# Kernel tuning notes

Hardware: AMD Instinct MI355X
Metric: run time of the kernel (lower is better)

## Reference

```python
import jax, jax.numpy as jnp
import numpy as np

N, E, H = 5000, 40000, 8
DIMS = [(258, 512), (516, 256), (262, 128), (136, 20)]  # (in_feature, out_feature) per GATDeformer


def setup_inputs() -> dict:
    key = jax.random.key(0)
    ks = jax.random.split(key, 10)
    s = 0.05
    data = jax.random.normal(ks[0], (N, 10), jnp.float32)
    src = jax.random.randint(ks[1], (E,), 0, N)
    off = jax.random.randint(ks[2], (E,), 1, N)
    edge_idx = jnp.stack([src, (src + off) % N]).astype(jnp.int32)  # no self loops by construction
    inp = {
        'data': data,
        'edge_idx': edge_idx,
        'W0': jax.random.normal(ks[3], (10, 256), jnp.float32) * s,
        'b0': jnp.zeros((256,), jnp.float32),
    }
    for i, (din, dout) in enumerate(DIMS, start=1):
        k = jax.random.split(ks[3 + i], 3)
        inp[f'W{i}'] = jax.random.normal(k[0], (din, H * dout), jnp.float32) * s
        inp[f'asrc{i}'] = jax.random.normal(k[1], (H, dout), jnp.float32) * s
        inp[f'adst{i}'] = jax.random.normal(k[2], (H, dout), jnp.float32) * s
        inp[f'bias{i}'] = jnp.zeros((dout,), jnp.float32)
    return inp


def _gat(x, src, dst, W, a_s, a_d, b):
    """PyG GATConv (concat=False): returns (mean-over-heads output + bias, alpha [E',H])."""
    Hh, C = a_s.shape
    h = (x @ W).reshape(N, Hh, C)                               # [N,H,C]
    e_s = jnp.einsum('nhc,hc->nh', h, a_s)                      # [N,H]
    e_d = jnp.einsum('nhc,hc->nh', h, a_d)
    logits = jax.nn.leaky_relu(e_s[src] + e_d[dst], 0.2)        # [E',H]
    m = jax.ops.segment_max(logits, dst, num_segments=N)        # segment softmax over incoming edges
    ex = jnp.exp(logits - m[dst])
    alpha = ex / jax.ops.segment_sum(ex, dst, num_segments=N)[dst]
    out = jax.ops.segment_sum(alpha[:, :, None] * h[src], dst, num_segments=N)  # [N,H,C]
    return out.mean(axis=1) + b, alpha


def _deformer(af, src, dst, W, a_s, a_d, b):
    # find_boundary on the layer input features
    up, down = af[:, 0] == 1.0, af[:, 0] == 0.0
    left, right = af[:, 1] == 0.0, af[:, 1] == 1.0
    feat, alpha = _gat(af, src, dst, W, a_s, a_d, b)
    coord = af[:, :2]
    # second propagate: alpha*0.2 reused to aggregate source coordinates, then mean over heads
    msg = (alpha * 0.2)[:, :, None] * coord[src][:, None, :]    # [E',H,2]
    oc = jax.ops.segment_sum(msg, dst, num_segments=N).mean(axis=1)
    # fix_boundary (sequential overwrite order: up then down, left then right)
    c0 = jnp.where(down, 0.0, jnp.where(up, 1.0, oc[:, 0]))
    c1 = jnp.where(right, 1.0, jnp.where(left, 0.0, oc[:, 1]))
    return jnp.stack([c0, c1], axis=1), jax.nn.selu(feat)


def reference(data, edge_idx, W0, b0, W1, asrc1, adst1, bias1, W2, asrc2, adst2, bias2, W3, asrc3, adst3, bias3, W4, asrc4, adst4, bias4):
    sl = jnp.arange(N, dtype=edge_idx.dtype)
    src = jnp.concatenate([edge_idx[0], sl])   # GATConv add_self_loops=True
    dst = jnp.concatenate([edge_idx[1], sl])
    coord = data[:, :2]
    feat = jax.nn.selu(data @ W0 + b0)
    c1_, f1 = _deformer(jnp.concatenate([coord, feat], 1), src, dst, W1, asrc1, adst1, bias1)
    c2_, f2 = _deformer(jnp.concatenate([c1_, coord, f1], 1), src, dst, W2, asrc2, adst2, bias2)
    c3_, f3 = _deformer(jnp.concatenate([c2_, c1_, coord, f2], 1), src, dst, W3, asrc3, adst3, bias3)
    c4_, _ = _deformer(jnp.concatenate([c3_, c2_, c1_, coord, f3], 1), src, dst, W4, asrc4, adst4, bias4)
    return c4_
```

## Files before the change

### kernel.cpp

```cpp
#include <hip/hip_runtime.h>

#define N_NODES 5000
#define NH 8

typedef unsigned short u16;
typedef short bf16x8 __attribute__((ext_vector_type(8)));
typedef float f32x4 __attribute__((ext_vector_type(4)));

static __device__ __forceinline__ float selu_f(float x) {
    const float sc = 1.0507009873554805f;
    const float al = 1.6732632423543772f;
    return x > 0.f ? sc * x : sc * al * (__expf(x) - 1.f);
}

static __device__ __forceinline__ u16 f2bf(float x) {
    union { float f; unsigned u; } v; v.f = x;
    unsigned r = v.u + 0x7fff + ((v.u >> 16) & 1);
    return (u16)(r >> 16);
}

static __device__ __forceinline__ float bf2f(unsigned hi16) {
    union { unsigned u; float f; } v; v.u = hi16 << 16;
    return v.f;
}

#define GL2LDS16(gp, lp)                                                        \
    __builtin_amdgcn_global_load_lds(                                           \
        (const __attribute__((address_space(1))) void*)(gp),                    \
        (__attribute__((address_space(3))) void*)(lp), 16, 0, 0)

__global__ void k_count(const int* __restrict__ ei, int* cnt, int E, int Esz) {
    int e = blockIdx.x * 256 + threadIdx.x;
    if (e >= Esz) return;
    int dst = (e < E) ? ei[E + e] : (e - E);
    atomicAdd(&cnt[dst], 1);
}

__global__ void k_scan(const int* __restrict__ cnt, int* __restrict__ rowp, int n) {
    __shared__ int ps[256];
    int t = threadIdx.x;
    int per = (n + 255) / 256;
    int b = t * per;
    int s = 0;
    for (int i = 0; i < per; ++i) { int idx = b + i; if (idx < n) s += cnt[idx]; }
    ps[t] = s;
    __syncthreads();
    for (int off = 1; off < 256; off <<= 1) {
        int v = (t >= off) ? ps[t - off] : 0;
        __syncthreads();
        ps[t] += v;
        __syncthreads();
    }
    int run = (t == 0) ? 0 : ps[t - 1];
    for (int i = 0; i < per; ++i) {
        int idx = b + i;
        if (idx < n) { rowp[idx] = run; run += cnt[idx]; }
    }
    if (t == 255) rowp[n] = run;
}

__global__ void k_fill(const int* __restrict__ ei, const int* __restrict__ rowp,
                       int* cur, int* ssrc, int E, int Esz) {
    int e = blockIdx.x * 256 + threadIdx.x;
    if (e >= Esz) return;
    int src, dst;
    if (e < E) { src = ei[e]; dst = ei[E + e]; }
    else       { src = e - E; dst = src; }
    int pos = rowp[dst] + atomicAdd(&cur[dst], 1);
    ssrc[pos] = src;
}

__global__ __launch_bounds__(256) void k_prep(
        const float* W1, const float* W2, const float* W3, const float* W4,
        const float* s1, const float* s2, const float* s3, const float* s4,
        const float* d1, const float* d2, const float* d3, const float* d4,
        float* __restrict__ fsAll, float* __restrict__ fdAll,
        u16* T1, u16* T2, u16* T3) {
    const int Ks[4] = {258, 516, 262, 136};
    const int Cs[4] = {512, 256, 128, 20};
    int bid = blockIdx.x;
    if (bid < 516) {
        int li = bid / 129;
        int k = (bid % 129) * 4 + (threadIdx.x >> 6);
        int lane = threadIdx.x & 63;
        if (k >= Ks[li]) return;
        const float* W  = (li == 0) ? W1 : (li == 1) ? W2 : (li == 2) ? W3 : W4;
        const float* as = (li == 0) ? s1 : (li == 1) ? s2 : (li == 2) ? s3 : s4;
        const float* ad = (li == 0) ? d1 : (li == 1) ? d2 : (li == 2) ? d3 : d4;
        int C = Cs[li];
        float s[8] = {0.f,0.f,0.f,0.f,0.f,0.f,0.f,0.f};
        float d[8] = {0.f,0.f,0.f,0.f,0.f,0.f,0.f,0.f};
        const float* wr = W + (size_t)k * 8 * C;
        for (int c = lane; c < C; c += 64) {
            #pragma unroll
            for (int h = 0; h < 8; ++h) {
                float w = wr[h * C + c];
                s[h] += w * as[h * C + c];
                d[h] += w * ad[h * C + c];
            }
        }
        #pragma unroll
        for (int off = 32; off >= 1; off >>= 1) {
            #pragma unroll
            for (int h = 0; h < 8; ++h) {
                s[h] += __shfl_xor(s[h], off);
                d[h] += __shfl_xor(d[h], off);
            }
        }
        if (lane == 0) {
            float* fo = fsAll + (size_t)li * 516 * 8 + k * 8;
            float* go = fdAll + (size_t)li * 516 * 8 + k * 8;
            #pragma unroll
            for (int h = 0; h < 8; ++h) { fo[h] = s[h]; go[h] = d[h]; }
        }
    } else {
        const int Kps[3] = {288, 544, 288};
        int w = bid - 516;
        int li = w / (16 * 136);
        int rem = w % (16 * 136);
        int c0 = (rem % 16) * 32;
        int j0 = (rem / 16) * 32;
        int C = Cs[li], K = Ks[li], Kp = Kps[li], KK = 8 * Kp;
        if (c0 >= C || j0 >= KK) return;
        const float* W = (li == 0) ? W1 : (li == 1) ? W2 : W3;
        u16* Wt2 = (li == 0) ? T1 : (li == 1) ? T2 : T3;
        __shared__ float tile[32][33];
        int h = j0 / Kp, k0 = j0 % Kp;
        int tid = threadIdx.x;
        for (int idx = tid; idx < 1024; idx += 256) {
            int kr = idx >> 5, cc = idx & 31;
            int gk = k0 + kr;
            tile[kr][cc] = (gk < K) ? W[(size_t)gk * (8 * C) + h * C + c0 + cc] : 0.f;
        }
        __syncthreads();
        for (int idx = tid; idx < 1024; idx += 256) {
            int cr = idx >> 5, kc = idx & 31;
            Wt2[(size_t)(c0 + cr) * KK + j0 + kc] = f2bf(tile[kc][cr]);
        }
    }
}

__global__ __launch_bounds__(256) void k_mf(const float* p0, const float* p1,
                                            const float* p2, const float* p3, int np,
                                            const float* __restrict__ data,
                                            const float* __restrict__ W0,
                                            const float* __restrict__ b0,
                                            const u16* __restrict__ facc,
                                            const float* __restrict__ biasp,
                                            int split, int MN, int FC, int K, int Kp,
                                            const float* __restrict__ fs,
                                            const float* __restrict__ fd,
                                            u16* __restrict__ afb,
                                            float* __restrict__ es, float* __restrict__ ed,
                                            float* __restrict__ c0out) {
    int n = blockIdx.x, t = threadIdx.x;
    __shared__ float drow[10];
    bool l1 = (biasp == nullptr);
    if (l1 && t < 10) drow[t] = data[n * 10 + t];
    __syncthreads();
    float pes[8] = {0.f,0.f,0.f,0.f,0.f,0.f,0.f,0.f};
    float ped[8] = {0.f,0.f,0.f,0.f,0.f,0.f,0.f,0.f};
    u16* rowb = afb + (size_t)n * Kp;
    for (int cf = t; cf < FC; cf += 256) {
        float v;
        if (l1) {
            v = b0[cf];
            #pragma unroll
            for (int k = 0; k < 10; ++k) v += drow[k] * W0[k * 256 + cf];
            v = selu_f(v);
        } else {
            float s = 0.f;
            for (int z = 0; z < split; ++z)
                s += bf2f(facc[(size_t)z * MN + (size_t)n * FC + cf]);
            v = selu_f(s * 0.125f + biasp[cf]);
        }
        int c = 2 * np + cf;
        rowb[c] = f2bf(v);
        const float* fsr = fs + c * 8;
        const float* fdr = fd + c * 8;
        #pragma unroll
        for (int h = 0; h < 8; ++h) { pes[h] += v * fsr[h]; ped[h] += v * fdr[h]; }
    }
    if (t < 2 * np) {
        float v;
        if (l1) {
            v = drow[t];
            c0out[n * 2 + t] = v;
        } else {
            const float* p = (t < 2) ? p0 : (t < 4) ? p1 : (t < 6) ? p2 : p3;
            v = p[n * 2 + (t & 1)];
        }
        rowb[t] = f2bf(v);
        #pragma unroll
        for (int h = 0; h < 8; ++h) { pes[h] += v * fs[t * 8 + h]; ped[h] += v * fd[t * 8 + h]; }
    }
    for (int c = K + t; c < Kp; c += 256) rowb[c] = 0;
    #pragma unroll
    for (int off = 32; off >= 1; off >>= 1) {
        #pragma unroll
        for (int h = 0; h < 8; ++h) {
            pes[h] += __shfl_xor(pes[h], off);
            ped[h] += __shfl_xor(ped[h], off);
        }
    }
    __shared__ float red[4][16];
    int wv = t >> 6, ln = t & 63;
    if (ln == 0) {
        #pragma unroll
        for (int h = 0; h < 8; ++h) { red[wv][h] = pes[h]; red[wv][8 + h] = ped[h]; }
    }
    __syncthreads();
    if (t < 16) {
        float s = red[0][t] + red[1][t] + red[2][t] + red[3][t];
        if (t < 8) es[n * 8 + t] = s;
        else       ed[n * 8 + (t - 8)] = s;
    }
}

template <int S32>
__global__ __launch_bounds__(256) void k_gag(const float* __restrict__ es,
                            const float* __restrict__ ed,
                            const int* __restrict__ rowp, const int* __restrict__ ssrc,
                            const float* __restrict__ cprev, const u16* __restrict__ afb,
                            u16* __restrict__ g, float* __restrict__ cnext, int Kp) {
    __shared__ int   ls[128];
    __shared__ float la[128 * 8];
    __shared__ float lc0[128], lc1[128], lw[128];
    __shared__ float linv[8];
    int n = blockIdx.x, t = threadIdx.x;
    int s0 = rowp[n];
    int deg = rowp[n + 1] - s0;
    if (deg > 128) deg = 128;
    for (int i = t; i < deg; i += 256) {
        int src = ssrc[s0 + i];
        ls[i] = src;
        lc0[i] = cprev[src * 2];
        lc1[i] = cprev[src * 2 + 1];
    }
    __syncthreads();
    for (int i = t; i < deg * 8; i += 256) {
        int e = i >> 3, h = i & 7;
        float x = es[ls[e] * 8 + h] + ed[n * 8 + h];
        la[i] = x > 0.f ? x : 0.2f * x;
    }
    __syncthreads();
    if (t < 8) {
        float m = -1e30f;
        for (int e = 0; e < deg; ++e) m = fmaxf(m, la[e * 8 + t]);
        float s = 0.f;
        for (int e = 0; e < deg; ++e) {
            float v = __expf(la[e * 8 + t] - m);
            la[e * 8 + t] = v;
            s += v;
        }
        linv[t] = 1.f / s;
    }
    __syncthreads();
    for (int i = t; i < deg; i += 256) {
        float w = 0.f;
        #pragma unroll
        for (int h = 0; h < 8; ++h) w += la[i * 8 + h] * linv[h];
        lw[i] = w;
    }
    int nW = Kp >> 1;
    float acc[8][2 * S32];
    #pragma unroll
    for (int h = 0; h < 8; ++h)
        #pragma unroll
        for (int s = 0; s < 2 * S32; ++s) acc[h][s] = 0.f;
    int e = 0;
    for (; e + 1 < deg; e += 2) {
        const unsigned* r0 = (const unsigned*)(afb + (size_t)ls[e] * Kp);
        const unsigned* r1 = (const unsigned*)(afb + (size_t)ls[e + 1] * Kp);
        unsigned v0[S32], v1[S32];
        #pragma unroll
        for (int s = 0; s < S32; ++s) {
            int w = t + 256 * s;
            v0[s] = (w < nW) ? r0[w] : 0u;
            v1[s] = (w < nW) ? r1[w] : 0u;
        }
        float a0[8], a1[8];
        #pragma unroll
        for (int h = 0; h < 8; ++h) { a0[h] = la[e * 8 + h]; a1[h] = la[(e + 1) * 8 + h]; }
        #pragma unroll
        for (int s = 0; s < S32; ++s) {
            float x0 = bf2f(v0[s] & 0xffff), y0 = bf2f(v0[s] >> 16);
            float x1 = bf2f(v1[s] & 0xffff), y1 = bf2f(v1[s] >> 16);
            #pragma unroll
            for (int h = 0; h < 8; ++h) {
                acc[h][2 * s]     += a0[h] * x0 + a1[h] * x1;
                acc[h][2 * s + 1] += a0[h] * y0 + a1[h] * y1;
            }
        }
    }
    if (e < deg) {
        const unsigned* r0 = (const unsigned*)(afb + (size_t)ls[e] * Kp);
        unsigned v0[S32];
        #pragma unroll
        for (int s = 0; s < S32; ++s) {
            int w = t + 256 * s;
            v0[s] = (w < nW) ? r0[w] : 0u;
        }
        float a0[8];
        #pragma unroll
        for (int h = 0; h < 8; ++h) a0[h] = la[e * 8 + h];
        #pragma unroll
        for (int s = 0; s < S32; ++s) {
            float x0 = bf2f(v0[s] & 0xffff), y0 = bf2f(v0[s] >> 16);
            #pragma unroll
            for (int h = 0; h < 8; ++h) {
                acc[h][2 * s]     += a0[h] * x0;
                acc[h][2 * s + 1] += a0[h] * y0;
            }
        }
    }
    unsigned* grw = (unsigned*)(g + (size_t)n * 8 * Kp);
    #pragma unroll
    for (int s = 0; s < S32; ++s) {
        int w = t + 256 * s;
        if (w < nW) {
            #pragma unroll
            for (int h = 0; h < 8; ++h) {
                float iv = linv[h];
                unsigned lo = f2bf(acc[h][2 * s] * iv);
                unsigned hi = f2bf(acc[h][2 * s + 1] * iv);
                grw[h * nW + w] = lo | (hi << 16);
            }
        }
    }
    __syncthreads();
    if (t == 0) {
        float oc0 = 0.f, oc1 = 0.f;
        for (int i = 0; i < deg; ++i) { oc0 += lw[i] * lc0[i]; oc1 += lw[i] * lc1[i]; }
        oc0 *= 0.025f; oc1 *= 0.025f;
        float a0 = cprev[n * 2], a1 = cprev[n * 2 + 1];
        cnext[n * 2]     = (a0 == 0.f) ? 0.f : ((a0 == 1.f) ? 1.f : oc0);
        cnext[n * 2 + 1] = (a1 == 1.f) ? 1.f : ((a1 == 0.f) ? 0.f : oc1);
    }
}

__global__ __launch_bounds__(256) void k_gemm_s(const u16* __restrict__ A,
                                                const u16* __restrict__ Bt,
                                                u16* __restrict__ facc16,
                                                int M, int KK, int NC, int kchunk, int MN) {
    __shared__ u16 As[2][128 * 32];
    __shared__ u16 Bs[2][128 * 32];
    int tid = threadIdx.x;
    int wave = tid >> 6, lane = tid & 63;
    int bm = blockIdx.y * 128, bn = blockIdx.x * 128, z = blockIdx.z;
    int kbeg = z * kchunk, kend = min(KK, kbeg + kchunk);
    int wm = (wave >> 1) * 64, wn = (wave & 1) * 64;
    int l16 = lane & 15, q = lane >> 4;
    f32x4 acc[4][4] = {};

    int seg0 = wave * 128 + lane;
    int seg1 = seg0 + 64;
    int row0 = seg0 >> 2, sq0 = (seg0 & 3) ^ (row0 & 3);
    int row1 = seg1 >> 2, sq1 = (seg1 & 3) ^ (row1 & 3);
    const u16* ga0 = A  + (size_t)(bm + row0) * KK + sq0 * 8;
    const u16* ga1 = A  + (size_t)(bm + row1) * KK + sq1 * 8;
    const u16* gb0 = Bt + (size_t)(bn + row0) * KK + sq0 * 8;
    const u16* gb1 = Bt + (size_t)(bn + row1) * KK + sq1 * 8;
    int lo0 = (wave * 2 + 0) * 512;
    int lo1 = (wave * 2 + 1) * 512;

#define STAGE_T(buf, kk)                          \
    do {                                          \
        GL2LDS16(ga0 + (kk), &As[buf][lo0]);      \
        GL2LDS16(ga1 + (kk), &As[buf][lo1]);      \
        GL2LDS16(gb0 + (kk), &Bs[buf][lo0]);      \
        GL2LDS16(gb1 + (kk), &Bs[buf][lo1]);      \
    } while (0)

    STAGE_T(0, kbeg);
    int cur = 0;
    for (int k0 = kbeg; k0 < kend; k0 += 32) {
        if (k0 + 32 < kend) {
            STAGE_T(cur ^ 1, k0 + 32);
            asm volatile("s_waitcnt vmcnt(4)" ::: "memory");
        } else {
            asm volatile("s_waitcnt vmcnt(0)" ::: "memory");
        }
        __builtin_amdgcn_s_barrier();
        const u16* Asr = As[cur];
        const u16* Bsr = Bs[cur];
        bf16x8 fa[4], fb[4];
        #pragma unroll
        for (int mi = 0; mi < 4; ++mi) {
            int row = wm + mi * 16 + l16;
            fa[mi] = *(const bf16x8*)(Asr + row * 32 + ((q ^ (row & 3)) * 8));
            int col = wn + mi * 16 + l16;
            fb[mi] = *(const bf16x8*)(Bsr + col * 32 + ((q ^ (col & 3)) * 8));
        }
        #pragma unroll
        for (int mi = 0; mi < 4; ++mi)
            #pragma unroll
            for (int ni = 0; ni < 4; ++ni)
                acc[mi][ni] = __builtin_amdgcn_mfma_f32_16x16x32_bf16(fa[mi], fb[ni], acc[mi][ni], 0, 0, 0);
        __builtin_amdgcn_s_barrier();
        cur ^= 1;
    }
#undef STAGE_T
    u16* out = facc16 + (size_t)z * MN;
    #pragma unroll
    for (int mi = 0; mi < 4; ++mi) {
        int row0s = bm + wm + mi * 16 + q * 4;
        #pragma unroll
        for (int ni = 0; ni < 4; ++ni) {
            int col = bn + wn + ni * 16 + l16;
            #pragma unroll
            for (int r = 0; r < 4; ++r) {
                int row = row0s + r;
                if (row < M) out[(size_t)row * NC + col] = f2bf(acc[mi][ni][r]);
            }
        }
    }
}

__global__ void k_final(const float* __restrict__ es, const float* __restrict__ ed,
                        const int* __restrict__ rowp, const int* __restrict__ ssrc,
                        const float* __restrict__ cprev, float* __restrict__ outp) {
    int wid = (blockIdx.x * blockDim.x + threadIdx.x) >> 6;
    int lane = threadIdx.x & 63;
    if (wid >= N_NODES) return;
    int n = wid;
    int s0 = rowp[n], deg = rowp[n + 1] - s0;
    int h = lane & 7, ei = lane >> 3;
    float edh = ed[n * 8 + h];
    float m = -1e30f;
    for (int b = 0; b < deg; b += 8) {
        int e = b + ei;
        if (e < deg) {
            int src = ssrc[s0 + e];
            float x = es[src * 8 + h] + edh;
            x = x > 0.f ? x : 0.2f * x;
            m = fmaxf(m, x);
        }
    }
    m = fmaxf(m, __shfl_xor(m, 8));
    m = fmaxf(m, __shfl_xor(m, 16));
    m = fmaxf(m, __shfl_xor(m, 32));
    float ssum = 0.f;
    for (int b = 0; b < deg; b += 8) {
        int e = b + ei;
        if (e < deg) {
            int src = ssrc[s0 + e];
            float x = es[src * 8 + h] + edh;
            x = x > 0.f ? x : 0.2f * x;
            ssum += __expf(x - m);
        }
    }
    ssum += __shfl_xor(ssum, 8);
    ssum += __shfl_xor(ssum, 16);
    ssum += __shfl_xor(ssum, 32);
    float inv = 1.f / ssum;
    float oc0 = 0.f, oc1 = 0.f;
    for (int b = 0; b < deg; b += 8) {
        int e = b + ei;
        if (e < deg) {
            int src = ssrc[s0 + e];
            float x = es[src * 8 + h] + edh;
            x = x > 0.f ? x : 0.2f * x;
            float w = __expf(x - m) * inv;
            w += __shfl_xor(w, 1);
            w += __shfl_xor(w, 2);
            w += __shfl_xor(w, 4);
            if (h == 0) {
                oc0 += w * cprev[src * 2];
                oc1 += w * cprev[src * 2 + 1];
            }
        }
    }
    oc0 += __shfl_xor(oc0, 8);  oc1 += __shfl_xor(oc1, 8);
    oc0 += __shfl_xor(oc0, 16); oc1 += __shfl_xor(oc1, 16);
    oc0 += __shfl_xor(oc0, 32); oc1 += __shfl_xor(oc1, 32);
    if (lane == 0) {
        oc0 *= 0.025f; oc1 *= 0.025f;
        float a0 = cprev[n * 2], a1 = cprev[n * 2 + 1];
        outp[n * 2]     = (a0 == 0.f) ? 0.f : ((a0 == 1.f) ? 1.f : oc0);
        outp[n * 2 + 1] = (a1 == 1.f) ? 1.f : ((a1 == 0.f) ? 0.f : oc1);
    }
}

extern "C" void kernel_launch(void* const* d_in, const int* in_sizes, int n_in,
                              void* d_out, int out_size, void* d_ws, size_t ws_size,
                              hipStream_t stream) {
    const float* data = (const float*)d_in[0];
    const int* ei = (const int*)d_in[1];
    const float* W0 = (const float*)d_in[2];
    const float* b0 = (const float*)d_in[3];
    int E = in_sizes[1] / 2;
    int Esz = E + N_NODES;

    char* wp = (char*)d_ws;
    size_t off = 0;
    auto alloc = [&](size_t bytes) {
        void* p = wp + off;
        off += (bytes + 1023) & ~(size_t)1023;
        return p;
    };
    u16*   g     = (u16*)alloc((size_t)N_NODES * 8 * 576 * 2);
    u16*   T1    = (u16*)alloc((size_t)512 * 8 * 288 * 2);
    u16*   T2    = (u16*)alloc((size_t)256 * 8 * 544 * 2);
    u16*   T3    = (u16*)alloc((size_t)128 * 8 * 288 * 2);
    u16*   facc  = (u16*)alloc((size_t)8 * N_NODES * 512 * 2);
    u16*   afb   = (u16*)alloc((size_t)N_NODES * 576 * 2);
    float* es    = (float*)alloc((size_t)N_NODES * 8 * 4);
    float* ebd   = (float*)alloc((size_t)N_NODES * 8 * 4);
    float* fsAll = (float*)alloc((size_t)4 * 516 * 8 * 4);
    float* fdAll = (float*)alloc((size_t)4 * 516 * 8 * 4);
    float* c0    = (float*)alloc(N_NODES * 2 * 4);
    float* c1    = (float*)alloc(N_NODES * 2 * 4);
    float* c2    = (float*)alloc(N_NODES * 2 * 4);
    float* c3    = (float*)alloc(N_NODES * 2 * 4);
    int* cnt  = (int*)alloc(N_NODES * 2 * 4);
    int* cur  = cnt + N_NODES;
    int* rowp = (int*)alloc((N_NODES + 1) * 4);
    int* ssrc = (int*)alloc(Esz * 4);

    hipMemsetAsync(cnt, 0, N_NODES * 2 * 4, stream);
    int gE = (Esz + 255) / 256;
    k_count<<<gE, 256, 0, stream>>>(ei, cnt, E, Esz);
    k_scan<<<1, 256, 0, stream>>>(cnt, rowp, N_NODES);
    k_fill<<<gE, 256, 0, stream>>>(ei, rowp, cur, ssrc, E, Esz);

    struct LP { const float *W, *as, *ad, *bs; int K, C, split; };
    LP L[4] = {
        {(const float*)d_in[4],  (const float*)d_in[5],  (const float*)d_in[6],  (const float*)d_in[7],  258, 512, 4},
        {(const float*)d_in[8],  (const float*)d_in[9],  (const float*)d_in[10], (const float*)d_in[11], 516, 256, 8},
        {(const float*)d_in[12], (const float*)d_in[13], (const float*)d_in[14], (const float*)d_in[15], 262, 128, 8},
        {(const float*)d_in[16], (const float*)d_in[17], (const float*)d_in[18], (const float*)d_in[19], 136, 20, 1},
    };
    k_prep<<<516 + 16 * 136 * 3, 256, 0, stream>>>(
        L[0].W, L[1].W, L[2].W, L[3].W,
        L[0].as, L[1].as, L[2].as, L[3].as,
        L[0].ad, L[1].ad, L[2].ad, L[3].ad,
        fsAll, fdAll, T1, T2, T3);

    float* cbuf[4] = {c0, c1, c2, c3};
    u16* Tb[3] = {T1, T2, T3};
    int FC[4] = {256, 512, 256, 128};

    for (int li = 0; li < 4; ++li) {
        LP& lp = L[li];
        const float* p[4] = {nullptr, nullptr, nullptr, nullptr};
        for (int j = 0; j <= li; ++j) p[j] = cbuf[li - j];
        int Kp = ((lp.K + 31) / 32) * 32;
        int KK = 8 * Kp;
        const float* biasp = (li == 0) ? nullptr : L[li - 1].bs;
        int splitp = (li == 0) ? 1 : L[li - 1].split;
        int MNp = N_NODES * FC[li];
        const float* fs = fsAll + (size_t)li * 516 * 8;
        const float* fd = fdAll + (size_t)li * 516 * 8;

        k_mf<<<N_NODES, 256, 0, stream>>>(p[0], p[1], p[2], p[3], li + 1,
                                          data, W0, b0, facc, biasp, splitp, MNp, FC[li],
                                          lp.K, Kp, fs, fd, afb, es, ebd, c0);
        if (li < 3) {
            if ((Kp >> 1) <= 256)
                k_gag<1><<<N_NODES, 256, 0, stream>>>(es, ebd, rowp, ssrc, cbuf[li], afb,
                                                      g, cbuf[li + 1], Kp);
            else
                k_gag<2><<<N_NODES, 256, 0, stream>>>(es, ebd, rowp, ssrc, cbuf[li], afb,
                                                      g, cbuf[li + 1], Kp);
            int MN = N_NODES * lp.C;
            k_gemm_s<<<dim3(lp.C / 128, (N_NODES + 127) / 128, lp.split), 256, 0, stream>>>(
                g, Tb[li], facc, N_NODES, KK, lp.C, KK / lp.split, MN);
        } else {
            k_final<<<(N_NODES + 3) / 4, 256, 0, stream>>>(es, ebd, rowp, ssrc, cbuf[3],
                                                           (float*)d_out);
        }
    }
}
```

Before: 369.8 us.

## Triple-buffer GEMM LDS, unroll aggregation by four edges, vectorize feature prep

The GEMM now keeps three LDS stages in flight instead of two, prefetching two k-steps ahead with adjusted vmcnt waits to better hide global-to-LDS latency. The edge aggregation loop processes four neighbor rows per iteration instead of two, raising memory-level parallelism, and the tail becomes a scalar loop. The feature-prep kernel handles two columns per thread with float2/packed bf16 loads and stores. These cost more LDS (lower occupancy risk) and more registers in the aggregation kernel.

```diff
diff --git a/kernel.cpp b/kernel.cpp
--- a/kernel.cpp
+++ b/kernel.cpp
@@ -161,25 +161,39 @@
     float pes[8] = {0.f,0.f,0.f,0.f,0.f,0.f,0.f,0.f};
     float ped[8] = {0.f,0.f,0.f,0.f,0.f,0.f,0.f,0.f};
     u16* rowb = afb + (size_t)n * Kp;
-    for (int cf = t; cf < FC; cf += 256) {
-        float v;
+    for (int cf2 = t; 2 * cf2 < FC; cf2 += 256) {
+        int cf = 2 * cf2;
+        float v0, v1;
         if (l1) {
-            v = b0[cf];
-            #pragma unroll
-            for (int k = 0; k < 10; ++k) v += drow[k] * W0[k * 256 + cf];
-            v = selu_f(v);
+            float2 bb = *(const float2*)(b0 + cf);
+            v0 = bb.x; v1 = bb.y;
+            #pragma unroll
+            for (int k = 0; k < 10; ++k) {
+                float2 ww = *(const float2*)(W0 + k * 256 + cf);
+                v0 += drow[k] * ww.x;
+                v1 += drow[k] * ww.y;
+            }
+            v0 = selu_f(v0); v1 = selu_f(v1);
         } else {
-            float s = 0.f;
-            for (int z = 0; z < split; ++z)
-                s += bf2f(facc[(size_t)z * MN + (size_t)n * FC + cf]);
-            v = selu_f(s * 0.125f + biasp[cf]);
+            float s0 = 0.f, s1 = 0.f;
+            for (int z = 0; z < split; ++z) {
+                unsigned pr = *(const unsigned*)(facc + (size_t)z * MN + (size_t)n * FC + cf);
+                s0 += bf2f(pr & 0xffff);
+                s1 += bf2f(pr >> 16);
+            }
+            float2 bb = *(const float2*)(biasp + cf);
+            v0 = selu_f(s0 * 0.125f + bb.x);
+            v1 = selu_f(s1 * 0.125f + bb.y);
         }
         int c = 2 * np + cf;
-        rowb[c] = f2bf(v);
+        *(unsigned*)(rowb + c) = (unsigned)f2bf(v0) | ((unsigned)f2bf(v1) << 16);
         const float* fsr = fs + c * 8;
         const float* fdr = fd + c * 8;
         #pragma unroll
-        for (int h = 0; h < 8; ++h) { pes[h] += v * fsr[h]; ped[h] += v * fdr[h]; }
+        for (int h = 0; h < 8; ++h) {
+            pes[h] += v0 * fsr[h] + v1 * fsr[8 + h];
+            ped[h] += v0 * fdr[h] + v1 * fdr[8 + h];
+        }
     }
     if (t < 2 * np) {
         float v;
@@ -269,31 +283,43 @@
         #pragma unroll
         for (int s = 0; s < 2 * S32; ++s) acc[h][s] = 0.f;
     int e = 0;
-    for (; e + 1 < deg; e += 2) {
+    for (; e + 3 < deg; e += 4) {
         const unsigned* r0 = (const unsigned*)(afb + (size_t)ls[e] * Kp);
         const unsigned* r1 = (const unsigned*)(afb + (size_t)ls[e + 1] * Kp);
-        unsigned v0[S32], v1[S32];
+        const unsigned* r2 = (const unsigned*)(afb + (size_t)ls[e + 2] * Kp);
+        const unsigned* r3 = (const unsigned*)(afb + (size_t)ls[e + 3] * Kp);
+        unsigned v0[S32], v1[S32], v2[S32], v3[S32];
         #pragma unroll
         for (int s = 0; s < S32; ++s) {
             int w = t + 256 * s;
-            v0[s] = (w < nW) ? r0[w] : 0u;
-            v1[s] = (w < nW) ? r1[w] : 0u;
-        }
-        float a0[8], a1[8];
-        #pragma unroll
-        for (int h = 0; h < 8; ++h) { a0[h] = la[e * 8 + h]; a1[h] = la[(e + 1) * 8 + h]; }
+            bool ok = (w < nW);
+            v0[s] = ok ? r0[w] : 0u;
+            v1[s] = ok ? r1[w] : 0u;
+            v2[s] = ok ? r2[w] : 0u;
+            v3[s] = ok ? r3[w] : 0u;
+        }
+        float a0[8], a1[8], a2[8], a3[8];
+        #pragma unroll
+        for (int h = 0; h < 8; ++h) {
+            a0[h] = la[(e + 0) * 8 + h];
+            a1[h] = la[(e + 1) * 8 + h];
+            a2[h] = la[(e + 2) * 8 + h];
+            a3[h] = la[(e + 3) * 8 + h];
+        }
         #pragma unroll
         for (int s = 0; s < S32; ++s) {
             float x0 = bf2f(v0[s] & 0xffff), y0 = bf2f(v0[s] >> 16);
             float x1 = bf2f(v1[s] & 0xffff), y1 = bf2f(v1[s] >> 16);
+            float x2 = bf2f(v2[s] & 0xffff), y2 = bf2f(v2[s] >> 16);
+            float x3 = bf2f(v3[s] & 0xffff), y3 = bf2f(v3[s] >> 16);
             #pragma unroll
             for (int h = 0; h < 8; ++h) {
-                acc[h][2 * s]     += a0[h] * x0 + a1[h] * x1;
-                acc[h][2 * s + 1] += a0[h] * y0 + a1[h] * y1;
-            }
-        }
-    }
-    if (e < deg) {
+                acc[h][2 * s]     += a0[h] * x0 + a1[h] * x1 + a2[h] * x2 + a3[h] * x3;
+                acc[h][2 * s + 1] += a0[h] * y0 + a1[h] * y1 + a2[h] * y2 + a3[h] * y3;
+            }
+        }
+    }
+    for (; e < deg; ++e) {
         const unsigned* r0 = (const unsigned*)(afb + (size_t)ls[e] * Kp);
         unsigned v0[S32];
         #pragma unroll
@@ -343,8 +369,8 @@
                                                 const u16* __restrict__ Bt,
                                                 u16* __restrict__ facc16,
                                                 int M, int KK, int NC, int kchunk, int MN) {
-    __shared__ u16 As[2][128 * 32];
-    __shared__ u16 Bs[2][128 * 32];
+    __shared__ u16 As[3][128 * 32];
+    __shared__ u16 Bs[3][128 * 32];
     int tid = threadIdx.x;
     int wave = tid >> 6, lane = tid & 63;
     int bm = blockIdx.y * 128, bn = blockIdx.x * 128, z = blockIdx.z;
@@ -373,10 +399,14 @@
     } while (0)
 
     STAGE_T(0, kbeg);
+    if (kbeg + 32 < kend) STAGE_T(1, kbeg + 32);
     int cur = 0;
     for (int k0 = kbeg; k0 < kend; k0 += 32) {
-        if (k0 + 32 < kend) {
-            STAGE_T(cur ^ 1, k0 + 32);
+        if (k0 + 64 < kend) {
+            int nb = cur + 2; if (nb >= 3) nb -= 3;
+            STAGE_T(nb, k0 + 64);
+            asm volatile("s_waitcnt vmcnt(8)" ::: "memory");
+        } else if (k0 + 32 < kend) {
             asm volatile("s_waitcnt vmcnt(4)" ::: "memory");
         } else {
             asm volatile("s_waitcnt vmcnt(0)" ::: "memory");
@@ -398,7 +428,7 @@
             for (int ni = 0; ni < 4; ++ni)
                 acc[mi][ni] = __builtin_amdgcn_mfma_f32_16x16x32_bf16(fa[mi], fb[ni], acc[mi][ni], 0, 0, 0);
         __builtin_amdgcn_s_barrier();
-        cur ^= 1;
+        cur += 1; if (cur >= 3) cur -= 3;
     }
 #undef STAGE_T
     u16* out = facc16 + (size_t)z * MN;
```

Measured after the change: 363.2 us. About the same (-1.8%).
